# Optimization experiments

Hardware: AMD Instinct MI355X
Metric: run time of the kernel (lower is better)

The kernel has to match this reference:

```python
import jax, jax.numpy as jnp
import numpy as np

GAMMA = 1.0

def setup_inputs() -> dict:
    key = jax.random.key(0)
    k1, k2, k3, k4 = jax.random.split(key, 4)
    B, C, H, W = 8192, 1, 48, 48
    output = jax.random.normal(k1, (B, C, H, W), dtype=jnp.float32)
    target = jax.random.normal(k2, (B, C, H, W), dtype=jnp.float32)
    psu = jax.random.normal(k3, (6, 9, H, W), dtype=jnp.float32)
    mu = jax.random.uniform(k4, (6, 9), dtype=jnp.float32)
    return {"output": output, "target": target, "psu": psu, "mu": mu}

def reference(output, target, psu, mu):
    # MSE term
    diff = output - target                      # [B,1,H,W]
    loss = jnp.mean(diff * diff)
    # |output*psu_ij - target*psu_ij| = |diff| * |psu_ij| (elementwise), so the
    # per-(i,j) L1 mean factorizes: mean_{b,c,h,w}(|diff|*|p|) = mean_{h,w}(A*|p|)
    # where A = mean_{b,c}|diff|. This fuses all 54 tiny torch kernels.
    H, W = output.shape[-2], output.shape[-1]
    A = jnp.mean(jnp.abs(diff), axis=(0, 1))    # [H,W]
    l1 = jnp.einsum('hw,ijhw->ij', A, jnp.abs(psu)) / (H * W)  # [6,n_shear]
    loss = loss + GAMMA * jnp.sum(mu * l1 * l1) / 2.0
    return loss
```

## Files before the change

kernel.cpp:

```cpp
#include <hip/hip_runtime.h>

#define HW 2304
#define HW4 576
#define PART_STRIDE 2308

__global__ __launch_bounds__(576) void sc_stage1(
    const float4* __restrict__ out4, const float4* __restrict__ tgt4,
    float* __restrict__ part, int B, int NB)
{
    int tid = threadIdx.x;
    int blk = blockIdx.x;
    float a0 = 0.f, a1 = 0.f, a2 = 0.f, a3 = 0.f, sq = 0.f;
    for (int b = blk; b < B; b += NB) {
        size_t base = (size_t)b * HW4 + tid;
        float4 o = out4[base];
        float4 t = tgt4[base];
        float d0 = o.x - t.x, d1 = o.y - t.y, d2 = o.z - t.z, d3 = o.w - t.w;
        sq = fmaf(d0, d0, sq);
        sq = fmaf(d1, d1, sq);
        sq = fmaf(d2, d2, sq);
        sq = fmaf(d3, d3, sq);
        a0 += fabsf(d0); a1 += fabsf(d1); a2 += fabsf(d2); a3 += fabsf(d3);
    }
    float* pbase = part + (size_t)blk * PART_STRIDE;
    ((float4*)pbase)[tid] = make_float4(a0, a1, a2, a3);

    #pragma unroll
    for (int off = 32; off; off >>= 1) sq += __shfl_down(sq, off);
    __shared__ float wsum[9];
    int wid = tid >> 6;
    if ((tid & 63) == 0) wsum[wid] = sq;
    __syncthreads();
    if (tid == 0) {
        float s = 0.f;
        #pragma unroll
        for (int w = 0; w < 9; ++w) s += wsum[w];
        pbase[HW] = s;
    }
}

__global__ __launch_bounds__(1024) void sc_stage2(
    const float* __restrict__ part, float* __restrict__ A,
    float* __restrict__ out, int NB, int B, float invN)
{
    __shared__ float red[16][64];
    int lane = threadIdx.x & 63;
    int grp  = threadIdx.x >> 6;
    int blk  = blockIdx.x;
    if (blk < 36) {
        int hw = blk * 64 + lane;
        float s = 0.f;
        for (int r = grp; r < NB; r += 16)
            s += part[(size_t)r * PART_STRIDE + hw];
        red[grp][lane] = s;
        __syncthreads();
        if (grp == 0) {
            float t = 0.f;
            #pragma unroll
            for (int g = 0; g < 16; ++g) t += red[g][lane];
            A[hw] = t / (float)B;
        }
    } else {
        float s = (threadIdx.x < NB)
                    ? part[(size_t)threadIdx.x * PART_STRIDE + HW] : 0.f;
        #pragma unroll
        for (int off = 32; off; off >>= 1) s += __shfl_down(s, off);
        if ((threadIdx.x & 63) == 0) red[0][grp] = s;
        __syncthreads();
        if (threadIdx.x == 0) {
            float t = 0.f;
            #pragma unroll
            for (int g = 0; g < 16; ++g) t += red[0][g];
            out[0] = t * invN;
        }
    }
}

__global__ __launch_bounds__(256) void sc_stage3(
    const float* __restrict__ A, const float* __restrict__ psu,
    const float* __restrict__ mu, float* __restrict__ out)
{
    int j = blockIdx.x;
    int tid = threadIdx.x;
    const float* p = psu + (size_t)j * HW;
    float s = 0.f;
    for (int hw = tid; hw < HW; hw += 256) s += A[hw] * fabsf(p[hw]);
    #pragma unroll
    for (int off = 32; off; off >>= 1) s += __shfl_down(s, off);
    __shared__ float wsum[4];
    if ((tid & 63) == 0) wsum[tid >> 6] = s;
    __syncthreads();
    if (tid == 0) {
        float l1 = (wsum[0] + wsum[1] + wsum[2] + wsum[3]) * (1.0f / HW);
        float contrib = 0.5f * mu[j] * l1 * l1;
        atomicAdd(out, contrib);
    }
}

extern "C" void kernel_launch(void* const* d_in, const int* in_sizes, int n_in,
                              void* d_out, int out_size, void* d_ws, size_t ws_size,
                              hipStream_t stream)
{
    const float* outp = (const float*)d_in[0];
    const float* tgtp = (const float*)d_in[1];
    const float* psu  = (const float*)d_in[2];
    const float* mu   = (const float*)d_in[3];

    int B   = in_sizes[0] / HW;
    int nij = in_sizes[3];

    int NB = 512;
    while (NB > 16 &&
           ((size_t)NB * PART_STRIDE + HW) * sizeof(float) > ws_size)
        NB >>= 1;

    float* part = (float*)d_ws;
    float* A    = part + (size_t)NB * PART_STRIDE;
    float invN  = 1.0f / ((float)B * (float)HW);

    sc_stage1<<<NB, 576, 0, stream>>>((const float4*)outp, (const float4*)tgtp,
                                      part, B, NB);
    sc_stage2<<<37, 1024, 0, stream>>>(part, A, (float*)d_out, NB, B, invN);
    sc_stage3<<<nij, 256, 0, stream>>>(A, psu, mu, (float*)d_out);
}
```

Before: 42.74 us.

## Flatten stage1 to grid-stride over elements with shared-memory atomic accumulation

Stage 1 now walks the flattened float4 array with 512-thread blocks instead of one thread per spatial position with 576 threads. Because a thread's spatial index now changes each iteration, per-position |diff| sums go into a shared-memory array through atomicAdd and are written out at the end. The aim is a block size that is a power of two with better occupancy and a fully flat, coalesced stream. The cost is four LDS atomics per float4, which may contend and slow the memory-bound loop. The minimum NB also changes.

```diff
diff --git a/kernel.cpp b/kernel.cpp
--- a/kernel.cpp
+++ b/kernel.cpp
@@ -3,38 +3,51 @@
 #define HW 2304
 #define HW4 576
 #define PART_STRIDE 2308
+#define S1_T 512
 
-__global__ __launch_bounds__(576) void sc_stage1(
+__global__ __launch_bounds__(S1_T, 8) void sc_stage1(
     const float4* __restrict__ out4, const float4* __restrict__ tgt4,
-    float* __restrict__ part, int B, int NB)
+    float* __restrict__ part, int N4, int step, int pstep)
 {
+    __shared__ float As[4][HW4];
+    __shared__ float wsum[8];
     int tid = threadIdx.x;
     int blk = blockIdx.x;
-    float a0 = 0.f, a1 = 0.f, a2 = 0.f, a3 = 0.f, sq = 0.f;
-    for (int b = blk; b < B; b += NB) {
-        size_t base = (size_t)b * HW4 + tid;
-        float4 o = out4[base];
-        float4 t = tgt4[base];
+
+    for (int k = tid; k < 4 * HW4; k += S1_T) (&As[0][0])[k] = 0.f;
+    __syncthreads();
+
+    float sq = 0.f;
+    int i = blk * S1_T + tid;
+    int p = i % HW4;
+    for (; i < N4; i += step) {
+        float4 o = out4[i];
+        float4 t = tgt4[i];
         float d0 = o.x - t.x, d1 = o.y - t.y, d2 = o.z - t.z, d3 = o.w - t.w;
         sq = fmaf(d0, d0, sq);
         sq = fmaf(d1, d1, sq);
         sq = fmaf(d2, d2, sq);
         sq = fmaf(d3, d3, sq);
-        a0 += fabsf(d0); a1 += fabsf(d1); a2 += fabsf(d2); a3 += fabsf(d3);
+        atomicAdd(&As[0][p], fabsf(d0));
+        atomicAdd(&As[1][p], fabsf(d1));
+        atomicAdd(&As[2][p], fabsf(d2));
+        atomicAdd(&As[3][p], fabsf(d3));
+        p += pstep; if (p >= HW4) p -= HW4;
     }
+    __syncthreads();
+
     float* pbase = part + (size_t)blk * PART_STRIDE;
-    ((float4*)pbase)[tid] = make_float4(a0, a1, a2, a3);
+    for (int k = tid; k < HW; k += S1_T)
+        pbase[k] = As[k & 3][k >> 2];
 
     #pragma unroll
     for (int off = 32; off; off >>= 1) sq += __shfl_down(sq, off);
-    __shared__ float wsum[9];
-    int wid = tid >> 6;
-    if ((tid & 63) == 0) wsum[wid] = sq;
+    if ((tid & 63) == 0) wsum[tid >> 6] = sq;
     __syncthreads();
     if (tid == 0) {
         float s = 0.f;
         #pragma unroll
-        for (int w = 0; w < 9; ++w) s += wsum[w];
+        for (int w = 0; w < 8; ++w) s += wsum[w];
         pbase[HW] = s;
     }
 }
@@ -108,9 +121,10 @@
 
     int B   = in_sizes[0] / HW;
     int nij = in_sizes[3];
+    int N4  = in_sizes[0] / 4;
 
     int NB = 512;
-    while (NB > 16 &&
+    while (NB > 64 &&
            ((size_t)NB * PART_STRIDE + HW) * sizeof(float) > ws_size)
         NB >>= 1;
 
@@ -118,8 +132,11 @@
     float* A    = part + (size_t)NB * PART_STRIDE;
     float invN  = 1.0f / ((float)B * (float)HW);
 
-    sc_stage1<<<NB, 576, 0, stream>>>((const float4*)outp, (const float4*)tgtp,
-                                      part, B, NB);
+    int step  = NB * S1_T;
+    int pstep = step % HW4;
+
+    sc_stage1<<<NB, S1_T, 0, stream>>>((const float4*)outp, (const float4*)tgtp,
+                                       part, N4, step, pstep);
     sc_stage2<<<37, 1024, 0, stream>>>(part, A, (float*)d_out, NB, B, invN);
     sc_stage3<<<nij, 256, 0, stream>>>(A, psu, mu, (float*)d_out);
 }
```

Result: slower. 117.2 us (+174.1%).

## Flatten stage-1 reduction into grid-stride loop with more, smaller blocks

Applied to the files above, without the earlier changes.

Stage 1 moves from one 576-thread block per batch slice to a flat grid-stride loop over all float4 elements. It now uses 256-thread blocks, 1152 blocks and nontemporal vector loads. Because the stride is a multiple of 576, each thread keeps a fixed spatial position, so the per-block partials are zero-filled first and then written at that position. The aim is better occupancy and less cache pollution on the streaming read. The cost is more partial rows: about twice the partial data to write and zero, and for stage 2's 37 blocks to read back.

```diff
diff --git a/kernel.cpp b/kernel.cpp
--- a/kernel.cpp
+++ b/kernel.cpp
@@ -3,40 +3,44 @@
 #define HW 2304
 #define HW4 576
 #define PART_STRIDE 2308
+#define S1_T 256
 
-__global__ __launch_bounds__(576) void sc_stage1(
-    const float4* __restrict__ out4, const float4* __restrict__ tgt4,
-    float* __restrict__ part, int B, int NB)
+typedef float __attribute__((ext_vector_type(4))) f32x4;
+
+__global__ __launch_bounds__(S1_T, 8) void sc_stage1(
+    const f32x4* __restrict__ out4, const f32x4* __restrict__ tgt4,
+    float* __restrict__ part, int N4, int NB)
 {
     int tid = threadIdx.x;
     int blk = blockIdx.x;
+    int stride = NB * S1_T;
+    int i0 = blk * S1_T + tid;
+    int p  = i0 % HW4;
+
     float a0 = 0.f, a1 = 0.f, a2 = 0.f, a3 = 0.f, sq = 0.f;
-    for (int b = blk; b < B; b += NB) {
-        size_t base = (size_t)b * HW4 + tid;
-        float4 o = out4[base];
-        float4 t = tgt4[base];
-        float d0 = o.x - t.x, d1 = o.y - t.y, d2 = o.z - t.z, d3 = o.w - t.w;
-        sq = fmaf(d0, d0, sq);
-        sq = fmaf(d1, d1, sq);
-        sq = fmaf(d2, d2, sq);
-        sq = fmaf(d3, d3, sq);
-        a0 += fabsf(d0); a1 += fabsf(d1); a2 += fabsf(d2); a3 += fabsf(d3);
+    for (int i = i0; i < N4; i += stride) {
+        f32x4 o = __builtin_nontemporal_load(&out4[i]);
+        f32x4 t = __builtin_nontemporal_load(&tgt4[i]);
+        float d;
+        d = o[0] - t[0]; sq = fmaf(d, d, sq); a0 += fabsf(d);
+        d = o[1] - t[1]; sq = fmaf(d, d, sq); a1 += fabsf(d);
+        d = o[2] - t[2]; sq = fmaf(d, d, sq); a2 += fabsf(d);
+        d = o[3] - t[3]; sq = fmaf(d, d, sq); a3 += fabsf(d);
     }
+
     float* pbase = part + (size_t)blk * PART_STRIDE;
-    ((float4*)pbase)[tid] = make_float4(a0, a1, a2, a3);
+    for (int k = tid; k < PART_STRIDE / 4; k += S1_T)
+        ((f32x4*)pbase)[k] = (f32x4){0.f, 0.f, 0.f, 0.f};
+    __syncthreads();
+    ((f32x4*)pbase)[p] = (f32x4){a0, a1, a2, a3};
 
     #pragma unroll
     for (int off = 32; off; off >>= 1) sq += __shfl_down(sq, off);
-    __shared__ float wsum[9];
-    int wid = tid >> 6;
-    if ((tid & 63) == 0) wsum[wid] = sq;
+    __shared__ float wsum[4];
+    if ((tid & 63) == 0) wsum[tid >> 6] = sq;
     __syncthreads();
-    if (tid == 0) {
-        float s = 0.f;
-        #pragma unroll
-        for (int w = 0; w < 9; ++w) s += wsum[w];
-        pbase[HW] = s;
-    }
+    if (tid == 0)
+        pbase[HW] = wsum[0] + wsum[1] + wsum[2] + wsum[3];
 }
 
 __global__ __launch_bounds__(1024) void sc_stage2(
@@ -61,8 +65,9 @@
             A[hw] = t / (float)B;
         }
     } else {
-        float s = (threadIdx.x < NB)
-                    ? part[(size_t)threadIdx.x * PART_STRIDE + HW] : 0.f;
+        float s = 0.f;
+        for (int k = threadIdx.x; k < NB; k += 1024)
+            s += part[(size_t)k * PART_STRIDE + HW];
         #pragma unroll
         for (int off = 32; off; off >>= 1) s += __shfl_down(s, off);
         if ((threadIdx.x & 63) == 0) red[0][grp] = s;
@@ -108,18 +113,18 @@
 
     int B   = in_sizes[0] / HW;
     int nij = in_sizes[3];
+    int N4  = in_sizes[0] / 4;
 
-    int NB = 512;
-    while (NB > 16 &&
-           ((size_t)NB * PART_STRIDE + HW) * sizeof(float) > ws_size)
-        NB >>= 1;
+    int NB = 1152;
+    if (((size_t)NB * PART_STRIDE + HW) * sizeof(float) > ws_size)
+        NB = 576;
 
     float* part = (float*)d_ws;
     float* A    = part + (size_t)NB * PART_STRIDE;
     float invN  = 1.0f / ((float)B * (float)HW);
 
-    sc_stage1<<<NB, 576, 0, stream>>>((const float4*)outp, (const float4*)tgtp,
-                                      part, B, NB);
+    sc_stage1<<<NB, S1_T, 0, stream>>>((const f32x4*)outp, (const f32x4*)tgtp,
+                                       part, N4, NB);
     sc_stage2<<<37, 1024, 0, stream>>>(part, A, (float*)d_out, NB, B, invN);
     sc_stage3<<<nij, 256, 0, stream>>>(A, psu, mu, (float*)d_out);
 }
```

Measured after the change: 58.42 us. 1.37x slower.
